# Kernel tuning notes

Measured on AMD Instinct MI355X. Metric: run time of the kernel, lower is better.

## Reference

```python
import jax, jax.numpy as jnp
import numpy as np

# ---- grid / physics constants (match init_kwargs) ----
B, K, NLAT, NLON = 1, 24, 721, 1440
R_EARTH = 6371000.0
R_GAS = 287.0
C_P = 1004.0
OMEGA = 7.292e-05
PHI_SURF = 0.0

_B_IF = np.linspace(1.0, 0.04, K + 1).astype(np.float32)   # interface b, level 0 = bottom
_A_IF = np.zeros(K + 1, dtype=np.float32)
B_MID = 0.5 * (_B_IF[1:] + _B_IF[:-1])
A_MID = 0.5 * (_A_IF[1:] + _A_IF[:-1])
DB = _B_IF[1:] - _B_IF[:-1]
DA = _A_IF[1:] - _A_IF[:-1]

_colat = np.linspace(0.0, np.pi, NLAT)
LATS = (np.pi / 2.0 - _colat).astype(np.float32)           # decreasing with index
COSLAT = np.clip(np.cos(LATS), 1e-3, None).astype(np.float32)
DTHETA = np.float32(np.pi / (NLAT - 1))
DLAM = np.float32(2.0 * np.pi / NLON)
F_COR = (2.0 * OMEGA * np.sin(LATS)).astype(np.float32)

_cos = jnp.asarray(COSLAT)[:, None]                         # (H,1), broadcasts over lon


def _dlam(x):
    # periodic centered difference along lon (last axis)
    return (jnp.roll(x, -1, -1) - jnp.roll(x, 1, -1)) / (2.0 * DLAM)


def _dphi(x):
    # d/d(latitude); lat index increases as latitude decreases -> minus sign
    c = (x[..., 2:, :] - x[..., :-2, :]) * 0.5
    t = x[..., 1:2, :] - x[..., 0:1, :]
    b = x[..., -1:, :] - x[..., -2:-1, :]
    return -jnp.concatenate([t, c, b], axis=-2) / DTHETA


def grad_s(s):
    # spherical gradient -> (..., H, W, 2): (zonal, meridional)
    return jnp.stack([_dlam(s) / (R_EARTH * _cos), _dphi(s) / R_EARTH], axis=-1)


def div_v(u, v):
    return (_dlam(u) + _dphi(v * _cos)) / (R_EARTH * _cos)


def curl_v(u, v):
    return (_dlam(v) - _dphi(u * _cos)) / (R_EARTH * _cos)


def setup_inputs() -> dict:
    key = jax.random.key(0)
    k1, k2, k3, k4 = jax.random.split(key, 4)
    uv = 10.0 * jax.random.normal(k1, (B, K, NLAT, NLON, 2), dtype=jnp.float32)
    T = 250.0 + 10.0 * jax.random.normal(k2, (B, K, NLAT, NLON), dtype=jnp.float32)
    q = 0.01 * jax.random.uniform(k3, (B, K, NLAT, NLON), dtype=jnp.float32)
    p_s = 9.0e4 + 1.0e4 * jax.random.uniform(k4, (B, NLAT, NLON), dtype=jnp.float32)
    return {"uv": uv, "T": T, "q": q, "p_s": p_s}


def reference(uv, T, q, p_s):
    am = jnp.asarray(A_MID)[None, :, None, None]
    bm = jnp.asarray(B_MID)[None, :, None, None]
    da = jnp.asarray(DA)[None, :, None, None]
    db = jnp.asarray(DB)[None, :, None, None]
    fcor = jnp.asarray(F_COR)[None, None, :, None]

    p = am + bm * p_s[:, None]           # (B,K,H,W) mid-level pressures
    dp = da + db * p_s[:, None]          # layer thicknesses
    u, v = uv[..., 0], uv[..., 1]

    # Block 1 outputs: vorticity, divergence per level (1/R-scaled spherical ops)
    zeta = curl_v(u, v)
    divg = div_v(u, v)
    ke = 0.5 * (u * u + v * v)

    # hydrostatic recurrence: phi_k = phi_{k-1} + R T_{k-1} ln(p_{k-1}/p_k)
    lr = jnp.log(p[:, :-1] / p[:, 1:])
    phi = PHI_SURF + jnp.concatenate(
        [jnp.zeros_like(p[:, :1]), jnp.cumsum(R_GAS * T[:, :-1] * lr, axis=1)], axis=1)

    gps = grad_s(p_s)                            # (B,H,W,2)
    vgps = u * gps[:, None, ..., 0] + v * gps[:, None, ..., 1]   # (B,K,H,W)

    # surface pressure tendency
    dpsdt = -jnp.sum(dp * divg + db * vgps, axis=1)              # (B,H,W)

    # C = (dp/deta) etadot at interfaces; bottom BC C_{-1/2}=0
    term = db * dpsdt[:, None] + dp * divg + db * vgps
    C_half = jnp.concatenate(
        [jnp.zeros_like(term[:, :1]), -jnp.cumsum(term, axis=1)], axis=1)  # (B,K+1,H,W)
    Cmid = 0.5 * (C_half[:, :-1] + C_half[:, 1:])

    # omega = Dp/Dt at mid levels
    omega_k = bm * (dpsdt[:, None] + vgps) + Cmid

    def ddp(X):
        # dX/dp: central interior, one-sided at top/bottom (matches _dX_dp)
        interior = (X[:, 2:] - X[:, :-2]) / (p[:, 2:] - p[:, :-2])
        top = (X[:, 1:2] - X[:, 0:1]) / (p[:, 1:2] - p[:, 0:1])
        bot = (X[:, -1:] - X[:, -2:-1]) / (p[:, -1:] - p[:, -2:-1])
        return jnp.concatenate([top, interior, bot], axis=1)

    g_kephi = grad_s(ke + phi)                   # -grad(KE) - grad(phi) combined
    abs_vort = zeta + fcor
    pgf_coef = R_GAS * T * bm / p                # PGF correction R T (dln p/dp_s) grad p_s

    du = abs_vort * v - g_kephi[..., 0] - pgf_coef * gps[:, None, ..., 0] - Cmid * ddp(u)
    dv = -abs_vort * u - g_kephi[..., 1] - pgf_coef * gps[:, None, ..., 1] - Cmid * ddp(v)

    gT = grad_s(T)
    gq = grad_s(q)
    dT = (-(u * gT[..., 0] + v * gT[..., 1]) - Cmid * ddp(T)
          + (R_GAS / C_P) * T * omega_k / p)
    dq = -(u * gq[..., 0] + v * gq[..., 1]) - Cmid * ddp(q)

    duv = jnp.stack([du, dv], axis=-1)
    return duv, dT, dq, dpsdt
```

## Files before the change

kernel.cpp:

```cpp
#include <hip/hip_runtime.h>
#include <math.h>

#define NLAT 721
#define NLON 1440
#define KLEV 24
#define S_LVL (NLAT * NLON)
#define WBLK 6
#define NBLK (WBLK * NLAT)

#define OFF_DT  (KLEV * S_LVL * 2)
#define OFF_DQ  (OFF_DT + KLEV * S_LVL)
#define OFF_DPS (OFF_DQ + KLEV * S_LVL)

__device__ __forceinline__ float BIF(int i) {
  if (i >= KLEV) return 0.04f;
  return (float)(1.0 + ((0.04 - 1.0) / 24.0) * (double)i);
}

__device__ __forceinline__ float latf(int i) {
  double colat = (i == NLAT - 1) ? M_PI : (M_PI / 720.0) * (double)i;
  return (float)(M_PI / 2.0 - colat);
}
__device__ __forceinline__ float coslatf(int i) {
  return fmaxf(cosf(latf(i)), 1e-3f);
}

__device__ __forceinline__ float dphi3(float xn, float xc, float xs, int h, float invdth) {
  float d = (h == 0) ? (xs - xc) : (h == NLAT - 1) ? (xc - xn) : (xs - xn) * 0.5f;
  return -d * invdth;
}

__device__ __forceinline__ void remap(int lb, int& h, int& w) {
  const int q = NBLK >> 3, r = NBLK & 7;
  int xcd = lb & 7, idx = lb >> 3;
  int wg = (xcd < r ? xcd * (q + 1) : r * (q + 1) + (xcd - r) * q) + idx;
  h = wg / WBLK;
  int bx = wg - h * WBLK;
  w = bx * 256 + (int)threadIdx.x;
}

__global__ __launch_bounds__(256) void kern_dpsdt(const float* __restrict__ uv,
                                                  const float* __restrict__ ps,
                                                  float* __restrict__ out) {
  int h, w;
  remap((int)blockIdx.x, h, w);
  if (w >= NLON) return;

  const int hN = (h > 0) ? h - 1 : 0;
  const int hS = (h < NLAT - 1) ? h + 1 : NLAT - 1;
  const int wE = (w == NLON - 1) ? 0 : w + 1;
  const int wW = (w == 0) ? NLON - 1 : w - 1;
  const int iC = h * NLON + w, iE = h * NLON + wE, iW = h * NLON + wW;
  const int iN = hN * NLON + w, iS = hS * NLON + w;

  const float cosC = coslatf(h), cosN = coslatf(hN), cosS = coslatf(hS);
  const float DLAM = (float)(2.0 * M_PI / 1440.0);
  const float DTHETA = (float)(M_PI / 720.0);
  const float inv2dlam = 1.0f / (2.0f * DLAM);
  const float invdth = 1.0f / DTHETA;
  const float invRcos = 1.0f / (6371000.0f * cosC);
  const float invR = 1.0f / 6371000.0f;

  const float psC = ps[iC], psE = ps[iE], psW = ps[iW], psN = ps[iN], psS = ps[iS];
  const float gpsx = (psE - psW) * inv2dlam * invRcos;
  const float gpsy = dphi3(psN, psC, psS, h, invdth) * invR;

  float acc = 0.0f;
  float bifc = 1.0f;
#pragma unroll 4
  for (int k = 0; k < KLEV; ++k) {
    const float* lvl = uv + (size_t)k * (size_t)(S_LVL * 2);
    const float2 c = *(const float2*)(lvl + 2 * iC);
    const float eu = lvl[2 * iE], wu = lvl[2 * iW];
    const float nv = lvl[2 * iN + 1], sv = lvl[2 * iS + 1];
    const float bifn = BIF(k + 1);
    const float db = bifn - bifc;
    bifc = bifn;
    float dlam_u = (eu - wu) * inv2dlam;
    float dphi_vc = dphi3(nv * cosN, c.y * cosC, sv * cosS, h, invdth);
    float divg = (dlam_u + dphi_vc) * invRcos;
    float vgps = c.x * gpsx + c.y * gpsy;
    float dp = db * psC;
    acc += dp * divg + db * vgps;
  }
  out[OFF_DPS + iC] = -acc;
}

__global__ __launch_bounds__(256) void kern_tend(const float* __restrict__ uv,
                                                 const float* __restrict__ Tf,
                                                 const float* __restrict__ qf,
                                                 const float* __restrict__ ps,
                                                 float* __restrict__ out) {
  int h, w;
  remap((int)blockIdx.x, h, w);
  if (w >= NLON) return;

  const int hN = (h > 0) ? h - 1 : 0;
  const int hS = (h < NLAT - 1) ? h + 1 : NLAT - 1;
  const int wE = (w == NLON - 1) ? 0 : w + 1;
  const int wW = (w == 0) ? NLON - 1 : w - 1;
  const int iC = h * NLON + w, iE = h * NLON + wE, iW = h * NLON + wW;
  const int iN = hN * NLON + w, iS = hS * NLON + w;

  const float cosC = coslatf(h), cosN = coslatf(hN), cosS = coslatf(hS);
  const float DLAM = (float)(2.0 * M_PI / 1440.0);
  const float DTHETA = (float)(M_PI / 720.0);
  const float inv2dlam = 1.0f / (2.0f * DLAM);
  const float invdth = 1.0f / DTHETA;
  const float invRcos = 1.0f / (6371000.0f * cosC);
  const float invR = 1.0f / 6371000.0f;
  const float KAPPA = (float)(287.0 / 1004.0);
  const float TWO_OMEGA = (float)(2.0 * 7.292e-05);
  const float fcor = TWO_OMEGA * sinf(latf(h));

  const float psC = ps[iC], psE = ps[iE], psW = ps[iW], psN = ps[iN], psS = ps[iS];
  const float gpsx = (psE - psW) * inv2dlam * invRcos;
  const float gpsy = dphi3(psN, psC, psS, h, invdth) * invR;

  const float dpsdt = out[OFF_DPS + iC];

  const float2* __restrict__ uv2 = (const float2*)uv;
  float2* duv2 = (float2*)out;

  float u_m1 = 0.f, v_m1 = 0.f, T_m1 = 0.f, q_m1 = 0.f;
  float2 c0 = uv2[iC];
  float u_0 = c0.x, v_0 = c0.y;
  float T_0 = Tf[iC], q_0 = qf[iC];
  float2 c1 = uv2[S_LVL + iC];
  float u_p1 = c1.x, v_p1 = c1.y;
  float T_p1 = Tf[S_LVL + iC], q_p1 = qf[S_LVL + iC];

  float phiC = 0.f, phiE = 0.f, phiW = 0.f, phiN = 0.f, phiS = 0.f;
  float TEp = 0.f, TWp = 0.f, TNp = 0.f, TSp = 0.f;
  float Chalf = 0.f;

  for (int m = 0; m < KLEV; ++m) {
    const int base = m * S_LVL;
    const float bifc = BIF(m), bifn = BIF(m + 1);
    const float db = bifn - bifc;
    const float bmC = 0.5f * (bifn + bifc);
    const float bmP = (m > 0) ? 0.5f * (bifc + BIF(m - 1)) : 0.f;
    const float bmN = (m < KLEV - 1) ? 0.5f * (BIF(m + 2) + bifn) : 0.f;

    float2 e = uv2[base + iE];
    float2 ww = uv2[base + iW];
    float2 n = uv2[base + iN];
    float2 s = uv2[base + iS];
    const float TE = Tf[base + iE], TW = Tf[base + iW], TN = Tf[base + iN], TS = Tf[base + iS];
    const float qE = qf[base + iE], qW = qf[base + iW], qN = qf[base + iN], qS = qf[base + iS];

    if (m > 0) {
      const float lr = logf(bmP / bmC);
      phiC += (287.0f * T_m1) * lr;
      phiE += (287.0f * TEp) * lr;
      phiW += (287.0f * TWp) * lr;
      phiN += (287.0f * TNp) * lr;
      phiS += (287.0f * TSp) * lr;
    }

    const float kC = 0.5f * (u_0 * u_0 + v_0 * v_0) + phiC;
    const float kE = 0.5f * (e.x * e.x + e.y * e.y) + phiE;
    const float kW = 0.5f * (ww.x * ww.x + ww.y * ww.y) + phiW;
    const float kN = 0.5f * (n.x * n.x + n.y * n.y) + phiN;
    const float kS = 0.5f * (s.x * s.x + s.y * s.y) + phiS;
    const float gkx = (kE - kW) * inv2dlam * invRcos;
    const float gky = dphi3(kN, kC, kS, h, invdth) * invR;

    const float zeta = ((e.y - ww.y) * inv2dlam -
                        dphi3(n.x * cosN, u_0 * cosC, s.x * cosS, h, invdth)) * invRcos;
    const float divg = ((e.x - ww.x) * inv2dlam +
                        dphi3(n.y * cosN, v_0 * cosC, s.y * cosS, h, invdth)) * invRcos;
    const float vgps = u_0 * gpsx + v_0 * gpsy;

    const float dp = db * psC;
    const float term = db * dpsdt + dp * divg + db * vgps;
    const float Cnext = Chalf - term;
    const float Cmid = 0.5f * (Chalf + Cnext);
    const float p_cur = bmC * psC;
    const float omega = bmC * (dpsdt + vgps) + Cmid;

    const float gTx = (TE - TW) * inv2dlam * invRcos;
    const float gTy = dphi3(TN, T_0, TS, h, invdth) * invR;
    const float gqx = (qE - qW) * inv2dlam * invRcos;
    const float gqy = dphi3(qN, q_0, qS, h, invdth) * invR;

    float num_u, num_v, num_T, num_q, dden;
    if (m == 0) {
      dden = bmN * psC - p_cur;
      num_u = u_p1 - u_0; num_v = v_p1 - v_0; num_T = T_p1 - T_0; num_q = q_p1 - q_0;
    } else if (m == KLEV - 1) {
      dden = p_cur - bmP * psC;
      num_u = u_0 - u_m1; num_v = v_0 - v_m1; num_T = T_0 - T_m1; num_q = q_0 - q_m1;
    } else {
      dden = bmN * psC - bmP * psC;
      num_u = u_p1 - u_m1; num_v = v_p1 - v_m1; num_T = T_p1 - T_m1; num_q = q_p1 - q_m1;
    }
    const float invdden = 1.0f / dden;
    const float ddpu = num_u * invdden;
    const float ddpv = num_v * invdden;
    const float ddpT = num_T * invdden;
    const float ddpq = num_q * invdden;

    const float invp = 1.0f / p_cur;
    const float pgf = (287.0f * T_0) * bmC * invp;
    const float av = zeta + fcor;

    const float du = ((av * v_0 - gkx) - pgf * gpsx) - Cmid * ddpu;
    const float dv = ((-av * u_0 - gky) - pgf * gpsy) - Cmid * ddpv;
    const float dTt = (-(u_0 * gTx + v_0 * gTy) - Cmid * ddpT) + ((KAPPA * T_0) * omega) * invp;
    const float dqt = -(u_0 * gqx + v_0 * gqy) - Cmid * ddpq;

    duv2[base + iC] = make_float2(du, dv);
    out[OFF_DT + base + iC] = dTt;
    out[OFF_DQ + base + iC] = dqt;

    Chalf = Cnext;
    TEp = TE; TWp = TW; TNp = TN; TSp = TS;
    u_m1 = u_0; v_m1 = v_0; T_m1 = T_0; q_m1 = q_0;
    u_0 = u_p1; v_0 = v_p1; T_0 = T_p1; q_0 = q_p1;
    if (m + 2 < KLEV) {
      const int bn = (m + 2) * S_LVL;
      float2 cn = uv2[bn + iC];
      u_p1 = cn.x; v_p1 = cn.y;
      T_p1 = Tf[bn + iC];
      q_p1 = qf[bn + iC];
    }
  }
}

extern "C" void kernel_launch(void* const* d_in, const int* in_sizes, int n_in,
                              void* d_out, int out_size, void* d_ws, size_t ws_size,
                              hipStream_t stream) {
  const float* uv = (const float*)d_in[0];
  const float* T  = (const float*)d_in[1];
  const float* q  = (const float*)d_in[2];
  const float* ps = (const float*)d_in[3];
  float* out = (float*)d_out;
  (void)in_sizes; (void)n_in; (void)out_size; (void)d_ws; (void)ws_size;

  dim3 grid(NBLK), block(256);
  hipLaunchKernelGGL(kern_dpsdt, grid, block, 0, stream, uv, ps, out);
  hipLaunchKernelGGL(kern_tend, grid, block, 0, stream, uv, T, q, ps, out);
}
```

Before: 829.3 us.

## Fuse surface-pressure tendency into main tendency kernel with precomputed level tables

Merges the two kernels into one: each thread first computes dpsdt over all levels and then immediately runs the tendency sweep. This removes the second launch and the write-then-read of dpsdt through global memory. Per-level constants (bm, db, 1/bm, 287·log ratio, ddp denominators) are now computed on the host and passed as a kernel argument, replacing per-thread logf and divisions. Outputs use nontemporal stores. The uv field is still read twice per thread, so the dpsdt pass sits on the critical path before the stores can start.

```diff
diff --git a/kernel.cpp b/kernel.cpp
--- a/kernel.cpp
+++ b/kernel.cpp
@@ -12,18 +12,21 @@
 #define OFF_DQ  (OFF_DT + KLEV * S_LVL)
 #define OFF_DPS (OFF_DQ + KLEV * S_LVL)
 
-__device__ __forceinline__ float BIF(int i) {
-  if (i >= KLEV) return 0.04f;
-  return (float)(1.0 + ((0.04 - 1.0) / 24.0) * (double)i);
-}
+typedef float f32x2 __attribute__((ext_vector_type(2)));
+
+struct Tabs {
+  float rlr[KLEV];
+  float bm[KLEV];
+  float db[KLEV];
+  float invbm[KLEV];
+  float dc[KLEV];
+};
 
 __device__ __forceinline__ float latf(int i) {
   double colat = (i == NLAT - 1) ? M_PI : (M_PI / 720.0) * (double)i;
   return (float)(M_PI / 2.0 - colat);
 }
-__device__ __forceinline__ float coslatf(int i) {
-  return fmaxf(cosf(latf(i)), 1e-3f);
-}
+__device__ __forceinline__ float coslatf(int i) { return fmaxf(cosf(latf(i)), 1e-3f); }
 
 __device__ __forceinline__ float dphi3(float xn, float xc, float xs, int h, float invdth) {
   float d = (h == 0) ? (xs - xc) : (h == NLAT - 1) ? (xc - xn) : (xs - xn) * 0.5f;
@@ -39,9 +42,11 @@
   w = bx * 256 + (int)threadIdx.x;
 }
 
-__global__ __launch_bounds__(256) void kern_dpsdt(const float* __restrict__ uv,
-                                                  const float* __restrict__ ps,
-                                                  float* __restrict__ out) {
+__global__ __launch_bounds__(256) void kern_fused(
+    const float* __restrict__ uv, const float* __restrict__ Tf,
+    const float* __restrict__ qf, const float* __restrict__ ps,
+    float* __restrict__ out, Tabs tb)
+{
   int h, w;
   remap((int)blockIdx.x, h, w);
   if (w >= NLON) return;
@@ -60,73 +65,39 @@
   const float invdth = 1.0f / DTHETA;
   const float invRcos = 1.0f / (6371000.0f * cosC);
   const float invR = 1.0f / 6371000.0f;
-
-  const float psC = ps[iC], psE = ps[iE], psW = ps[iW], psN = ps[iN], psS = ps[iS];
-  const float gpsx = (psE - psW) * inv2dlam * invRcos;
-  const float gpsy = dphi3(psN, psC, psS, h, invdth) * invR;
-
-  float acc = 0.0f;
-  float bifc = 1.0f;
-#pragma unroll 4
-  for (int k = 0; k < KLEV; ++k) {
-    const float* lvl = uv + (size_t)k * (size_t)(S_LVL * 2);
-    const float2 c = *(const float2*)(lvl + 2 * iC);
-    const float eu = lvl[2 * iE], wu = lvl[2 * iW];
-    const float nv = lvl[2 * iN + 1], sv = lvl[2 * iS + 1];
-    const float bifn = BIF(k + 1);
-    const float db = bifn - bifc;
-    bifc = bifn;
-    float dlam_u = (eu - wu) * inv2dlam;
-    float dphi_vc = dphi3(nv * cosN, c.y * cosC, sv * cosS, h, invdth);
-    float divg = (dlam_u + dphi_vc) * invRcos;
-    float vgps = c.x * gpsx + c.y * gpsy;
-    float dp = db * psC;
-    acc += dp * divg + db * vgps;
-  }
-  out[OFF_DPS + iC] = -acc;
-}
-
-__global__ __launch_bounds__(256) void kern_tend(const float* __restrict__ uv,
-                                                 const float* __restrict__ Tf,
-                                                 const float* __restrict__ qf,
-                                                 const float* __restrict__ ps,
-                                                 float* __restrict__ out) {
-  int h, w;
-  remap((int)blockIdx.x, h, w);
-  if (w >= NLON) return;
-
-  const int hN = (h > 0) ? h - 1 : 0;
-  const int hS = (h < NLAT - 1) ? h + 1 : NLAT - 1;
-  const int wE = (w == NLON - 1) ? 0 : w + 1;
-  const int wW = (w == 0) ? NLON - 1 : w - 1;
-  const int iC = h * NLON + w, iE = h * NLON + wE, iW = h * NLON + wW;
-  const int iN = hN * NLON + w, iS = hS * NLON + w;
-
-  const float cosC = coslatf(h), cosN = coslatf(hN), cosS = coslatf(hS);
-  const float DLAM = (float)(2.0 * M_PI / 1440.0);
-  const float DTHETA = (float)(M_PI / 720.0);
-  const float inv2dlam = 1.0f / (2.0f * DLAM);
-  const float invdth = 1.0f / DTHETA;
-  const float invRcos = 1.0f / (6371000.0f * cosC);
-  const float invR = 1.0f / 6371000.0f;
+  const float gxc = inv2dlam * invRcos;
   const float KAPPA = (float)(287.0 / 1004.0);
   const float TWO_OMEGA = (float)(2.0 * 7.292e-05);
   const float fcor = TWO_OMEGA * sinf(latf(h));
 
   const float psC = ps[iC], psE = ps[iE], psW = ps[iW], psN = ps[iN], psS = ps[iS];
-  const float gpsx = (psE - psW) * inv2dlam * invRcos;
+  const float invps = 1.0f / psC;
+  const float gpsx = (psE - psW) * gxc;
   const float gpsy = dphi3(psN, psC, psS, h, invdth) * invR;
 
-  const float dpsdt = out[OFF_DPS + iC];
-
-  const float2* __restrict__ uv2 = (const float2*)uv;
-  float2* duv2 = (float2*)out;
+  float acc = 0.0f;
+#pragma unroll 6
+  for (int k = 0; k < KLEV; ++k) {
+    const float* lvl = uv + (size_t)(2 * k) * (size_t)S_LVL;
+    const f32x2 c = *(const f32x2*)(lvl + 2 * iC);
+    const float eu = lvl[2 * iE], wu = lvl[2 * iW];
+    const float nv = lvl[2 * iN + 1], sv = lvl[2 * iS + 1];
+    float divg = (eu - wu) * gxc +
+                 dphi3(nv * cosN, c.y * cosC, sv * cosS, h, invdth) * invRcos;
+    float vgps = c.x * gpsx + c.y * gpsy;
+    acc += tb.db[k] * (psC * divg + vgps);
+  }
+  const float dpsdt = -acc;
+  __builtin_nontemporal_store(dpsdt, out + OFF_DPS + iC);
+
+  const f32x2* __restrict__ uv2 = (const f32x2*)uv;
+  f32x2* duv2 = (f32x2*)out;
 
   float u_m1 = 0.f, v_m1 = 0.f, T_m1 = 0.f, q_m1 = 0.f;
-  float2 c0 = uv2[iC];
+  f32x2 c0 = uv2[iC];
   float u_0 = c0.x, v_0 = c0.y;
   float T_0 = Tf[iC], q_0 = qf[iC];
-  float2 c1 = uv2[S_LVL + iC];
+  f32x2 c1 = uv2[S_LVL + iC];
   float u_p1 = c1.x, v_p1 = c1.y;
   float T_p1 = Tf[S_LVL + iC], q_p1 = qf[S_LVL + iC];
 
@@ -136,26 +107,23 @@
 
   for (int m = 0; m < KLEV; ++m) {
     const int base = m * S_LVL;
-    const float bifc = BIF(m), bifn = BIF(m + 1);
-    const float db = bifn - bifc;
-    const float bmC = 0.5f * (bifn + bifc);
-    const float bmP = (m > 0) ? 0.5f * (bifc + BIF(m - 1)) : 0.f;
-    const float bmN = (m < KLEV - 1) ? 0.5f * (BIF(m + 2) + bifn) : 0.f;
-
-    float2 e = uv2[base + iE];
-    float2 ww = uv2[base + iW];
-    float2 n = uv2[base + iN];
-    float2 s = uv2[base + iS];
+    const float bmC = tb.bm[m];
+    const float db = tb.db[m];
+
+    f32x2 e = uv2[base + iE];
+    f32x2 ww = uv2[base + iW];
+    f32x2 n = uv2[base + iN];
+    f32x2 s = uv2[base + iS];
     const float TE = Tf[base + iE], TW = Tf[base + iW], TN = Tf[base + iN], TS = Tf[base + iS];
     const float qE = qf[base + iE], qW = qf[base + iW], qN = qf[base + iN], qS = qf[base + iS];
 
     if (m > 0) {
-      const float lr = logf(bmP / bmC);
-      phiC += (287.0f * T_m1) * lr;
-      phiE += (287.0f * TEp) * lr;
-      phiW += (287.0f * TWp) * lr;
-      phiN += (287.0f * TNp) * lr;
-      phiS += (287.0f * TSp) * lr;
+      const float rlr = tb.rlr[m];
+      phiC += T_m1 * rlr;
+      phiE += TEp * rlr;
+      phiW += TWp * rlr;
+      phiN += TNp * rlr;
+      phiS += TSp * rlr;
     }
 
     const float kC = 0.5f * (u_0 * u_0 + v_0 * v_0) + phiC;
@@ -163,56 +131,50 @@
     const float kW = 0.5f * (ww.x * ww.x + ww.y * ww.y) + phiW;
     const float kN = 0.5f * (n.x * n.x + n.y * n.y) + phiN;
     const float kS = 0.5f * (s.x * s.x + s.y * s.y) + phiS;
-    const float gkx = (kE - kW) * inv2dlam * invRcos;
+    const float gkx = (kE - kW) * gxc;
     const float gky = dphi3(kN, kC, kS, h, invdth) * invR;
 
-    const float zeta = ((e.y - ww.y) * inv2dlam -
-                        dphi3(n.x * cosN, u_0 * cosC, s.x * cosS, h, invdth)) * invRcos;
-    const float divg = ((e.x - ww.x) * inv2dlam +
-                        dphi3(n.y * cosN, v_0 * cosC, s.y * cosS, h, invdth)) * invRcos;
+    const float zeta = (e.y - ww.y) * gxc -
+                       dphi3(n.x * cosN, u_0 * cosC, s.x * cosS, h, invdth) * invRcos;
+    const float divg = (e.x - ww.x) * gxc +
+                       dphi3(n.y * cosN, v_0 * cosC, s.y * cosS, h, invdth) * invRcos;
     const float vgps = u_0 * gpsx + v_0 * gpsy;
 
-    const float dp = db * psC;
-    const float term = db * dpsdt + dp * divg + db * vgps;
+    const float term = db * (dpsdt + psC * divg + vgps);
     const float Cnext = Chalf - term;
     const float Cmid = 0.5f * (Chalf + Cnext);
-    const float p_cur = bmC * psC;
     const float omega = bmC * (dpsdt + vgps) + Cmid;
-
-    const float gTx = (TE - TW) * inv2dlam * invRcos;
+    const float invp = tb.invbm[m] * invps;
+
+    const float gTx = (TE - TW) * gxc;
     const float gTy = dphi3(TN, T_0, TS, h, invdth) * invR;
-    const float gqx = (qE - qW) * inv2dlam * invRcos;
+    const float gqx = (qE - qW) * gxc;
     const float gqy = dphi3(qN, q_0, qS, h, invdth) * invR;
 
-    float num_u, num_v, num_T, num_q, dden;
+    float num_u, num_v, num_T, num_q;
     if (m == 0) {
-      dden = bmN * psC - p_cur;
       num_u = u_p1 - u_0; num_v = v_p1 - v_0; num_T = T_p1 - T_0; num_q = q_p1 - q_0;
     } else if (m == KLEV - 1) {
-      dden = p_cur - bmP * psC;
       num_u = u_0 - u_m1; num_v = v_0 - v_m1; num_T = T_0 - T_m1; num_q = q_0 - q_m1;
     } else {
-      dden = bmN * psC - bmP * psC;
       num_u = u_p1 - u_m1; num_v = v_p1 - v_m1; num_T = T_p1 - T_m1; num_q = q_p1 - q_m1;
     }
-    const float invdden = 1.0f / dden;
-    const float ddpu = num_u * invdden;
-    const float ddpv = num_v * invdden;
-    const float ddpT = num_T * invdden;
-    const float ddpq = num_q * invdden;
-
-    const float invp = 1.0f / p_cur;
-    const float pgf = (287.0f * T_0) * bmC * invp;
+    const float invdden = tb.dc[m] * invps;
+    const float CmidD = Cmid * invdden;
+
+    const float pgf = (287.0f * T_0) * invps;
     const float av = zeta + fcor;
 
-    const float du = ((av * v_0 - gkx) - pgf * gpsx) - Cmid * ddpu;
-    const float dv = ((-av * u_0 - gky) - pgf * gpsy) - Cmid * ddpv;
-    const float dTt = (-(u_0 * gTx + v_0 * gTy) - Cmid * ddpT) + ((KAPPA * T_0) * omega) * invp;
-    const float dqt = -(u_0 * gqx + v_0 * gqy) - Cmid * ddpq;
-
-    duv2[base + iC] = make_float2(du, dv);
-    out[OFF_DT + base + iC] = dTt;
-    out[OFF_DQ + base + iC] = dqt;
+    const float du = ((av * v_0 - gkx) - pgf * gpsx) - CmidD * num_u;
+    const float dv = ((-av * u_0 - gky) - pgf * gpsy) - CmidD * num_v;
+    const float dTt = (-(u_0 * gTx + v_0 * gTy) - CmidD * num_T)
+                      + ((KAPPA * T_0) * omega) * invp;
+    const float dqt = -(u_0 * gqx + v_0 * gqy) - CmidD * num_q;
+
+    f32x2 r; r.x = du; r.y = dv;
+    __builtin_nontemporal_store(r, duv2 + base + iC);
+    __builtin_nontemporal_store(dTt, out + OFF_DT + base + iC);
+    __builtin_nontemporal_store(dqt, out + OFF_DQ + base + iC);
 
     Chalf = Cnext;
     TEp = TE; TWp = TW; TNp = TN; TSp = TS;
@@ -220,7 +182,7 @@
     u_0 = u_p1; v_0 = v_p1; T_0 = T_p1; q_0 = q_p1;
     if (m + 2 < KLEV) {
       const int bn = (m + 2) * S_LVL;
-      float2 cn = uv2[bn + iC];
+      f32x2 cn = uv2[bn + iC];
       u_p1 = cn.x; v_p1 = cn.y;
       T_p1 = Tf[bn + iC];
       q_p1 = qf[bn + iC];
@@ -238,7 +200,24 @@
   float* out = (float*)d_out;
   (void)in_sizes; (void)n_in; (void)out_size; (void)d_ws; (void)ws_size;
 
-  dim3 grid(NBLK), block(256);
-  hipLaunchKernelGGL(kern_dpsdt, grid, block, 0, stream, uv, ps, out);
-  hipLaunchKernelGGL(kern_tend, grid, block, 0, stream, uv, T, q, ps, out);
-}
+  Tabs tb;
+  const double step = (0.04 - 1.0) / 24.0;
+  float bif[KLEV + 1];
+  for (int i = 0; i <= KLEV; ++i)
+    bif[i] = (i == KLEV) ? 0.04f : (float)(1.0 + step * (double)i);
+  float bm[KLEV];
+  for (int k = 0; k < KLEV; ++k) {
+    bm[k] = 0.5f * (bif[k + 1] + bif[k]);
+    tb.bm[k] = bm[k];
+    tb.db[k] = bif[k + 1] - bif[k];
+    tb.invbm[k] = 1.0f / bm[k];
+  }
+  tb.rlr[0] = 0.0f;
+  for (int m = 1; m < KLEV; ++m) tb.rlr[m] = 287.0f * logf(bm[m - 1] / bm[m]);
+  tb.dc[0] = 1.0f / (bm[1] - bm[0]);
+  tb.dc[KLEV - 1] = 1.0f / (bm[KLEV - 1] - bm[KLEV - 2]);
+  for (int m = 1; m < KLEV - 1; ++m) tb.dc[m] = 1.0f / (bm[m + 1] - bm[m - 1]);
+
+  hipLaunchKernelGGL(kern_fused, dim3(NBLK), dim3(256), 0, stream,
+                     uv, T, q, ps, out, tb);
+}
```

Result: faster. 812.0 us (-2.1%).
